# Performance work log

Measured on AMD Instinct MI355X. Metric: run time of the kernel, lower is better.

## Reference

```python
import jax, jax.numpy as jnp
import numpy as np

NUM_PATCHES = 16
FILTER_SIZE = 4
IN_CHANNELS = 64
OUT_CHANNELS = 256
BATCH = 64


def setup_inputs() -> dict:
    key = jax.random.key(0)
    k1, k2 = jax.random.split(key)
    D = NUM_PATCHES * FILTER_SIZE
    x = jax.random.normal(k1, (BATCH, IN_CHANNELS, D, D), dtype=jnp.float32)
    w = jax.random.normal(
        k2,
        (OUT_CHANNELS, IN_CHANNELS, NUM_PATCHES, NUM_PATCHES, FILTER_SIZE ** 2),
        dtype=jnp.float32,
    )
    return {"x": x, "w": w}


def reference(x, w):
    # x: (N, C, D, D) with D = P*f ; w: (O, C, P, P, f^2)
    N, C, D, _ = x.shape
    O, _, P, _, f2 = w.shape
    f = int(round(f2 ** 0.5))
    # non-overlapping unfold: (N,C,P,f,P,f) -> (N,C,P,P,f,f) -> (N,C,P,P,f^2)
    patches = x.reshape(N, C, P, f, P, f).transpose(0, 1, 2, 4, 3, 5).reshape(N, C, P, P, f2)
    # locally-connected contraction over in_channels and filter elements
    y = jnp.einsum('ncpqf,ocpqf->nopq', patches, w)
    scale = 1.0 / jnp.sqrt(jnp.asarray(f2 * C, dtype=x.dtype))
    return jax.nn.relu(y * scale)
```

## Files before the change

### kernel.cpp

```cpp
#include <hip/hip_runtime.h>


typedef short bf16x8 __attribute__((ext_vector_type(8)));
typedef float f32x4  __attribute__((ext_vector_type(4)));

__device__ __forceinline__ short f2bf(float f) {
    union { float f; unsigned u; } v; v.f = f;
    return (short)((v.u + 0x7FFFu + ((v.u >> 16) & 1u)) >> 16);
}

__device__ __forceinline__ bf16x8 pack8(f32x4 a, f32x4 b) {
    bf16x8 r;
    r[0] = f2bf(a[0]); r[1] = f2bf(a[1]); r[2] = f2bf(a[2]); r[3] = f2bf(a[3]);
    r[4] = f2bf(b[0]); r[5] = f2bf(b[1]); r[6] = f2bf(b[2]); r[7] = f2bf(b[3]);
    return r;
}

__device__ __forceinline__ void gload16(const void* g, void* l) {
    __builtin_amdgcn_global_load_lds(
        (const __attribute__((address_space(1))) void*)g,
        (__attribute__((address_space(3))) void*)l, 16, 0, 0);
}

__global__ __launch_bounds__(512)
void locblock_fused(const float* __restrict__ x, const float* __restrict__ w,
                    float* __restrict__ out) {
    __shared__ __align__(16) char smem[3][49152];

    const int hw = blockIdx.x;
    const int lb = (hw & 7) * 32 + (hw >> 3);
    const int p  = lb >> 4;
    const int q2 = (lb >> 1) & 7;
    const int oh = lb & 1;

    const int tid  = (int)threadIdx.x;
    const int lane = tid & 63;
    const int wv   = tid >> 6;
    const int l15  = lane & 15;
    const int kq   = lane >> 4;
    const int qw   = wv & 1;
    const int nc   = wv >> 1;

    const float* xsrc[2];
#pragma unroll
    for (int j = 0; j < 2; ++j) {
        const int id = j * 512 + tid;
        const int n = id >> 4, s = id & 15;
        const int u = s ^ (n & 15);
        xsrc[j] = x + (size_t)n * 262144u + (size_t)(u >> 3) * 4096u
                    + (size_t)(4 * p + ((u >> 1) & 3)) * 64u
                    + (size_t)(q2 * 8 + (u & 1) * 4);
    }
    const float* wsrc[4];
#pragma unroll
    for (int j = 0; j < 4; ++j) {
        const int id = j * 512 + tid;
        const int ol = id >> 4, s = id & 15;
        const int u = s ^ (ol & 15);
        wsrc[j] = w + (size_t)(oh * 128 + ol) * 262144u + (size_t)(u >> 3) * 4096u
                    + (size_t)p * 256u + (size_t)(q2 * 32) + (size_t)((u & 7) * 4);
    }

    int aoff[4][2], boff[2][2];
#pragma unroll
    for (int mf = 0; mf < 4; ++mf) {
        const int n = mf * 16 + l15;
        const int v1 = (kq >> 1) * 8 + (kq & 1) * 4 + qw;
        aoff[mf][0] = n * 256 + ((v1       ^ l15) * 16);
        aoff[mf][1] = n * 256 + (((v1 + 2) ^ l15) * 16);
    }
#pragma unroll
    for (int nf = 0; nf < 2; ++nf) {
        const int ol = nc * 32 + nf * 16 + l15;
        const int u1 = (kq >> 1) * 8 + qw * 4 + (kq & 1) * 2;
        boff[nf][0] = 16384 + ol * 256 + ((u1       ^ l15) * 16);
        boff[nf][1] = 16384 + ol * 256 + (((u1 + 1) ^ l15) * 16);
    }

    f32x4 acc[4][2];
#pragma unroll
    for (int mf = 0; mf < 4; ++mf)
#pragma unroll
        for (int nf = 0; nf < 2; ++nf)
            acc[mf][nf] = (f32x4){0.f, 0.f, 0.f, 0.f};

    auto stage = [&](int t, int buf) {
        char* base = smem[buf];
        const size_t toff = (size_t)t * 8192u;
#pragma unroll
        for (int j = 0; j < 2; ++j)
            gload16(xsrc[j] + toff, base + j * 8192 + wv * 1024);
#pragma unroll
        for (int j = 0; j < 4; ++j)
            gload16(wsrc[j] + toff, base + 16384 + j * 8192 + wv * 1024);
    };

    auto compute = [&](int buf) {
        const char* Lb = smem[buf];
        bf16x8 av[4], bv[2];
#pragma unroll
        for (int mf = 0; mf < 4; ++mf)
            av[mf] = pack8(*(const f32x4*)(Lb + aoff[mf][0]),
                           *(const f32x4*)(Lb + aoff[mf][1]));
#pragma unroll
        for (int nf = 0; nf < 2; ++nf)
            bv[nf] = pack8(*(const f32x4*)(Lb + boff[nf][0]),
                           *(const f32x4*)(Lb + boff[nf][1]));
#pragma unroll
        for (int mf = 0; mf < 4; ++mf)
#pragma unroll
            for (int nf = 0; nf < 2; ++nf)
                acc[mf][nf] = __builtin_amdgcn_mfma_f32_16x16x32_bf16(
                    av[mf], bv[nf], acc[mf][nf], 0, 0, 0);
    };

    stage(0, 0);
    stage(1, 1);
    stage(2, 2);
#pragma unroll 1
    for (int t = 0; t < 29; ++t) {
        const int buf = t % 3;
        asm volatile("s_waitcnt vmcnt(12)" ::: "memory");
        __builtin_amdgcn_s_barrier();
        compute(buf);
        asm volatile("s_waitcnt lgkmcnt(0)" ::: "memory");
        __builtin_amdgcn_s_barrier();
        stage(t + 3, buf);
    }
    asm volatile("s_waitcnt vmcnt(12)" ::: "memory");
    __builtin_amdgcn_s_barrier();
    compute(2);
    asm volatile("s_waitcnt vmcnt(6)" ::: "memory");
    __builtin_amdgcn_s_barrier();
    compute(0);
    asm volatile("s_waitcnt vmcnt(0)" ::: "memory");
    __builtin_amdgcn_s_barrier();
    compute(1);

    const float scale = 0.03125f;
    const int pq = p * 16 + q2 * 2 + qw;
#pragma unroll
    for (int mf = 0; mf < 4; ++mf)
#pragma unroll
        for (int nf = 0; nf < 2; ++nf) {
            const int o = oh * 128 + nc * 32 + nf * 16 + l15;
            float* ob = out + (size_t)(mf * 16 + kq * 4) * 65536u
                            + (size_t)o * 256u + pq;
#pragma unroll
            for (int j = 0; j < 4; ++j)
                ob[(size_t)j * 65536u] = fmaxf(acc[mf][nf][j] * scale, 0.0f);
        }
}

extern "C" void kernel_launch(void* const* d_in, const int* in_sizes, int n_in,
                              void* d_out, int out_size, void* d_ws, size_t ws_size,
                              hipStream_t stream) {
    const float* x = (const float*)d_in[0];
    const float* w = (const float*)d_in[1];
    float* out = (float*)d_out;
    locblock_fused<<<dim3(256), dim3(512), 0, stream>>>(x, w, out);
}
```

Before: 95.54 us.

## Retile locally-connected GEMM per patch row with f16 MFMA and LDS-staged output

Each block now handles one patch row p, 32 batch items and 32 output channels across all 16 q positions, instead of a (p, q-pair, o-half) tile. Inputs are loaded as contiguous 1 KB rows per (n or o, channel) into a double-buffered 64 KB LDS stage, iterating over all 64 channels. Each wave computes two q positions using f16 16x16x16 MFMA with a simple truncating conversion, replacing the bf16 16x16x32 path and its manual rounding. Results go through an LDS transpose so global stores become float4 writes contiguous in q. This trades a shallower pipeline and smaller per-wave tiles for more coalesced loads and stores, and f16 conversion could overflow for large inputs.

New measurement: 94.25 us. About the same (-1.4%).

```diff
diff --git a/kernel.cpp b/kernel.cpp
--- a/kernel.cpp
+++ b/kernel.cpp
@@ -1,20 +1,8 @@
 #include <hip/hip_runtime.h>
 
 
-typedef short bf16x8 __attribute__((ext_vector_type(8)));
-typedef float f32x4  __attribute__((ext_vector_type(4)));
-
-__device__ __forceinline__ short f2bf(float f) {
-    union { float f; unsigned u; } v; v.f = f;
-    return (short)((v.u + 0x7FFFu + ((v.u >> 16) & 1u)) >> 16);
-}
-
-__device__ __forceinline__ bf16x8 pack8(f32x4 a, f32x4 b) {
-    bf16x8 r;
-    r[0] = f2bf(a[0]); r[1] = f2bf(a[1]); r[2] = f2bf(a[2]); r[3] = f2bf(a[3]);
-    r[4] = f2bf(b[0]); r[5] = f2bf(b[1]); r[6] = f2bf(b[2]); r[7] = f2bf(b[3]);
-    return r;
-}
+typedef float    f32x4 __attribute__((ext_vector_type(4)));
+typedef _Float16 f16x4 __attribute__((ext_vector_type(4)));
 
 __device__ __forceinline__ void gload16(const void* g, void* l) {
     __builtin_amdgcn_global_load_lds(
@@ -22,134 +10,149 @@
         (__attribute__((address_space(3))) void*)l, 16, 0, 0);
 }
 
+__device__ __forceinline__ f16x4 cvt4(f32x4 v) {
+    f16x4 r;
+    r[0] = (_Float16)v[0]; r[1] = (_Float16)v[1];
+    r[2] = (_Float16)v[2]; r[3] = (_Float16)v[3];
+    return r;
+}
+
 __global__ __launch_bounds__(512)
 void locblock_fused(const float* __restrict__ x, const float* __restrict__ w,
                     float* __restrict__ out) {
-    __shared__ __align__(16) char smem[3][49152];
+    __shared__ __align__(16) char smem[131072];
 
     const int hw = blockIdx.x;
     const int lb = (hw & 7) * 32 + (hw >> 3);
     const int p  = lb >> 4;
-    const int q2 = (lb >> 1) & 7;
-    const int oh = lb & 1;
+    const int og = (lb >> 1) & 7;
+    const int nh = lb & 1;
 
     const int tid  = (int)threadIdx.x;
     const int lane = tid & 63;
     const int wv   = tid >> 6;
     const int l15  = lane & 15;
     const int kq   = lane >> 4;
-    const int qw   = wv & 1;
-    const int nc   = wv >> 1;
 
-    const float* xsrc[2];
-#pragma unroll
-    for (int j = 0; j < 2; ++j) {
-        const int id = j * 512 + tid;
-        const int n = id >> 4, s = id & 15;
-        const int u = s ^ (n & 15);
-        xsrc[j] = x + (size_t)n * 262144u + (size_t)(u >> 3) * 4096u
-                    + (size_t)(4 * p + ((u >> 1) & 3)) * 64u
-                    + (size_t)(q2 * 8 + (u & 1) * 4);
-    }
+    const int u = lane ^ wv;
+    const float* xsrc[4];
     const float* wsrc[4];
 #pragma unroll
     for (int j = 0; j < 4; ++j) {
-        const int id = j * 512 + tid;
-        const int ol = id >> 4, s = id & 15;
-        const int u = s ^ (ol & 15);
-        wsrc[j] = w + (size_t)(oh * 128 + ol) * 262144u + (size_t)(u >> 3) * 4096u
-                    + (size_t)p * 256u + (size_t)(q2 * 32) + (size_t)((u & 7) * 4);
+        xsrc[j] = x + (size_t)(nh * 32 + j * 8 + wv) * 262144u
+                    + (size_t)p * 256u + (size_t)(u * 4);
+        wsrc[j] = w + (size_t)(og * 32 + j * 8 + wv) * 262144u
+                    + (size_t)p * 256u + (size_t)(u * 4);
     }
 
-    int aoff[4][2], boff[2][2];
+    int aoff[2][2], boff[2][2];
 #pragma unroll
-    for (int mf = 0; mf < 4; ++mf) {
-        const int n = mf * 16 + l15;
-        const int v1 = (kq >> 1) * 8 + (kq & 1) * 4 + qw;
-        aoff[mf][0] = n * 256 + ((v1       ^ l15) * 16);
-        aoff[mf][1] = n * 256 + (((v1 + 2) ^ l15) * 16);
-    }
+    for (int qi = 0; qi < 2; ++qi) {
+        const int q = wv * 2 + qi;
 #pragma unroll
-    for (int nf = 0; nf < 2; ++nf) {
-        const int ol = nc * 32 + nf * 16 + l15;
-        const int u1 = (kq >> 1) * 8 + qw * 4 + (kq & 1) * 2;
-        boff[nf][0] = 16384 + ol * 256 + ((u1       ^ l15) * 16);
-        boff[nf][1] = 16384 + ol * 256 + (((u1 + 1) ^ l15) * 16);
+        for (int mf = 0; mf < 2; ++mf)
+            aoff[qi][mf] = (mf * 16 + l15) * 1024
+                         + (((kq * 16 + q) ^ (l15 & 7)) * 16);
+#pragma unroll
+        for (int nf = 0; nf < 2; ++nf)
+            boff[qi][nf] = 32768 + (nf * 16 + l15) * 1024
+                         + (((q * 4 + kq) ^ (l15 & 7)) * 16);
     }
 
-    f32x4 acc[4][2];
+    f32x4 acc[2][2][2];
 #pragma unroll
-    for (int mf = 0; mf < 4; ++mf)
+    for (int qi = 0; qi < 2; ++qi)
 #pragma unroll
-        for (int nf = 0; nf < 2; ++nf)
-            acc[mf][nf] = (f32x4){0.f, 0.f, 0.f, 0.f};
+        for (int mf = 0; mf < 2; ++mf)
+#pragma unroll
+            for (int nf = 0; nf < 2; ++nf)
+                acc[qi][mf][nf] = (f32x4){0.f, 0.f, 0.f, 0.f};
 
-    auto stage = [&](int t, int buf) {
-        char* base = smem[buf];
-        const size_t toff = (size_t)t * 8192u;
-#pragma unroll
-        for (int j = 0; j < 2; ++j)
-            gload16(xsrc[j] + toff, base + j * 8192 + wv * 1024);
+    auto stage = [&](int c) {
+        char* base = smem + (size_t)(c & 1) * 65536u;
+        const size_t coff = (size_t)c * 4096u;
 #pragma unroll
         for (int j = 0; j < 4; ++j)
-            gload16(wsrc[j] + toff, base + 16384 + j * 8192 + wv * 1024);
+            gload16(xsrc[j] + coff, base + (j * 8 + wv) * 1024);
+#pragma unroll
+        for (int j = 0; j < 4; ++j)
+            gload16(wsrc[j] + coff, base + 32768 + (j * 8 + wv) * 1024);
     };
 
-    auto compute = [&](int buf) {
-        const char* Lb = smem[buf];
-        bf16x8 av[4], bv[2];
+    auto compute = [&](int c) {
+        const char* base = smem + (size_t)(c & 1) * 65536u;
 #pragma unroll
-        for (int mf = 0; mf < 4; ++mf)
-            av[mf] = pack8(*(const f32x4*)(Lb + aoff[mf][0]),
-                           *(const f32x4*)(Lb + aoff[mf][1]));
+        for (int qi = 0; qi < 2; ++qi) {
+            f16x4 av[2], bv[2];
 #pragma unroll
-        for (int nf = 0; nf < 2; ++nf)
-            bv[nf] = pack8(*(const f32x4*)(Lb + boff[nf][0]),
-                           *(const f32x4*)(Lb + boff[nf][1]));
-#pragma unroll
-        for (int mf = 0; mf < 4; ++mf)
+            for (int mf = 0; mf < 2; ++mf)
+                av[mf] = cvt4(*(const f32x4*)(base + aoff[qi][mf]));
 #pragma unroll
             for (int nf = 0; nf < 2; ++nf)
-                acc[mf][nf] = __builtin_amdgcn_mfma_f32_16x16x32_bf16(
-                    av[mf], bv[nf], acc[mf][nf], 0, 0, 0);
+                bv[nf] = cvt4(*(const f32x4*)(base + boff[qi][nf]));
+#pragma unroll
+            for (int mf = 0; mf < 2; ++mf)
+#pragma unroll
+                for (int nf = 0; nf < 2; ++nf)
+                    acc[qi][mf][nf] = __builtin_amdgcn_mfma_f32_16x16x16f16(
+                        av[mf], bv[nf], acc[qi][mf][nf], 0, 0, 0);
+        }
     };
 
-    stage(0, 0);
-    stage(1, 1);
-    stage(2, 2);
+    stage(0);
+    stage(1);
 #pragma unroll 1
-    for (int t = 0; t < 29; ++t) {
-        const int buf = t % 3;
-        asm volatile("s_waitcnt vmcnt(12)" ::: "memory");
+    for (int c = 0; c < 62; ++c) {
+        asm volatile("s_waitcnt vmcnt(8)" ::: "memory");
         __builtin_amdgcn_s_barrier();
-        compute(buf);
+        compute(c);
         asm volatile("s_waitcnt lgkmcnt(0)" ::: "memory");
         __builtin_amdgcn_s_barrier();
-        stage(t + 3, buf);
+        stage(c + 2);
     }
-    asm volatile("s_waitcnt vmcnt(12)" ::: "memory");
+    asm volatile("s_waitcnt vmcnt(8)" ::: "memory");
     __builtin_amdgcn_s_barrier();
-    compute(2);
-    asm volatile("s_waitcnt vmcnt(6)" ::: "memory");
-    __builtin_amdgcn_s_barrier();
-    compute(0);
+    compute(62);
     asm volatile("s_waitcnt vmcnt(0)" ::: "memory");
     __builtin_amdgcn_s_barrier();
-    compute(1);
+    compute(63);
 
+    __syncthreads();
+
+    float* T = (float*)smem;
     const float scale = 0.03125f;
-    const int pq = p * 16 + q2 * 2 + qw;
 #pragma unroll
-    for (int mf = 0; mf < 4; ++mf)
+    for (int qi = 0; qi < 2; ++qi) {
+        const int q = wv * 2 + qi;
 #pragma unroll
-        for (int nf = 0; nf < 2; ++nf) {
-            const int o = oh * 128 + nc * 32 + nf * 16 + l15;
-            float* ob = out + (size_t)(mf * 16 + kq * 4) * 65536u
-                            + (size_t)o * 256u + pq;
+        for (int mf = 0; mf < 2; ++mf)
 #pragma unroll
-            for (int j = 0; j < 4; ++j)
-                ob[(size_t)j * 65536u] = fmaxf(acc[mf][nf][j] * scale, 0.0f);
-        }
+            for (int nf = 0; nf < 2; ++nf) {
+                f32x4 r;
+#pragma unroll
+                for (int j = 0; j < 4; ++j)
+                    r[j] = fmaxf(acc[qi][mf][nf][j] * scale, 0.0f);
+                *(f32x4*)(T + q * 1152 + (nf * 16 + l15) * 36
+                            + mf * 16 + kq * 4) = r;
+            }
+    }
+    __syncthreads();
+
+#pragma unroll
+    for (int i = 0; i < 8; ++i) {
+        const int item = i * 512 + tid;
+        const int o  = item >> 7;
+        const int rm = item & 127;
+        const int n  = rm >> 2;
+        const int qg = rm & 3;
+        f32x4 r;
+#pragma unroll
+        for (int s = 0; s < 4; ++s)
+            r[s] = T[(qg * 4 + s) * 1152 + o * 36 + n];
+        *(f32x4*)(out + (size_t)(nh * 32 + n) * 65536u
+                      + (size_t)(og * 32 + o) * 256u
+                      + (size_t)(p * 16 + qg * 4)) = r;
+    }
 }
 
 extern "C" void kernel_launch(void* const* d_in, const int* in_sizes, int n_in,
```

## Retile blocks to 4 q-positions x 64 outputs, double-buffer, stage epilogue via LDS

Applied to the files above, without the earlier changes.

Each block's tile changes from 2 q-positions x 128 output channels to 4 q-positions x 64 output channels. The x-tile per stage doubles while the w-tile stays the same size. The LDS pipeline drops from three buffers to two larger 64KB buffers, which shortens the prefetch depth. The epilogue now transposes results through LDS so each thread writes contiguous 16-byte float4 stores along q, replacing scattered scalar stores. This trades less pipelining depth and an extra LDS round-trip for coalesced output writes and a different x/w reuse balance.

Result: faster. 86.41 us (-9.6%).

```diff
diff --git a/kernel.cpp b/kernel.cpp
--- a/kernel.cpp
+++ b/kernel.cpp
@@ -25,56 +25,61 @@
 __global__ __launch_bounds__(512)
 void locblock_fused(const float* __restrict__ x, const float* __restrict__ w,
                     float* __restrict__ out) {
-    __shared__ __align__(16) char smem[3][49152];
+    __shared__ __align__(16) char smem[131072];
 
     const int hw = blockIdx.x;
     const int lb = (hw & 7) * 32 + (hw >> 3);
     const int p  = lb >> 4;
-    const int q2 = (lb >> 1) & 7;
-    const int oh = lb & 1;
+    const int q4 = (lb >> 2) & 3;
+    const int oq = lb & 3;
 
     const int tid  = (int)threadIdx.x;
     const int lane = tid & 63;
     const int wv   = tid >> 6;
     const int l15  = lane & 15;
     const int kq   = lane >> 4;
-    const int qw   = wv & 1;
-    const int nc   = wv >> 1;
+    const int qiw  = wv >> 1;
+    const int ow   = wv & 1;
 
-    const float* xsrc[2];
+    const float* xsrc[4];
 #pragma unroll
-    for (int j = 0; j < 2; ++j) {
+    for (int j = 0; j < 4; ++j) {
         const int id = j * 512 + tid;
-        const int n = id >> 4, s = id & 15;
+        const int n = id >> 5, s = id & 31;
         const int u = s ^ (n & 15);
-        xsrc[j] = x + (size_t)n * 262144u + (size_t)(u >> 3) * 4096u
-                    + (size_t)(4 * p + ((u >> 1) & 3)) * 64u
-                    + (size_t)(q2 * 8 + (u & 1) * 4);
+        xsrc[j] = x + (size_t)n * 262144u + (size_t)(u >> 4) * 4096u
+                    + (size_t)(4 * p + ((u >> 2) & 3)) * 64u
+                    + (size_t)(q4 * 16 + (u & 3) * 4);
     }
     const float* wsrc[4];
 #pragma unroll
     for (int j = 0; j < 4; ++j) {
         const int id = j * 512 + tid;
-        const int ol = id >> 4, s = id & 15;
-        const int u = s ^ (ol & 15);
-        wsrc[j] = w + (size_t)(oh * 128 + ol) * 262144u + (size_t)(u >> 3) * 4096u
-                    + (size_t)p * 256u + (size_t)(q2 * 32) + (size_t)((u & 7) * 4);
+        const int o = id >> 5, s = id & 31;
+        const int u = s ^ (o & 15);
+        wsrc[j] = w + (size_t)(oq * 64 + o) * 262144u + (size_t)(u >> 4) * 4096u
+                    + (size_t)p * 256u + (size_t)(q4 * 64) + (size_t)((u & 15) * 4);
     }
 
     int aoff[4][2], boff[2][2];
+    {
+        const int coff = kq >> 1, fr0 = (kq & 1) * 2;
 #pragma unroll
-    for (int mf = 0; mf < 4; ++mf) {
-        const int n = mf * 16 + l15;
-        const int v1 = (kq >> 1) * 8 + (kq & 1) * 4 + qw;
-        aoff[mf][0] = n * 256 + ((v1       ^ l15) * 16);
-        aoff[mf][1] = n * 256 + (((v1 + 2) ^ l15) * 16);
-    }
+        for (int mf = 0; mf < 4; ++mf) {
+            const int n = mf * 16 + l15;
 #pragma unroll
-    for (int nf = 0; nf < 2; ++nf) {
-        const int ol = nc * 32 + nf * 16 + l15;
-        const int u1 = (kq >> 1) * 8 + qw * 4 + (kq & 1) * 2;
-        boff[nf][0] = 16384 + ol * 256 + ((u1       ^ l15) * 16);
-        boff[nf][1] = 16384 + ol * 256 + (((u1 + 1) ^ l15) * 16);
+            for (int d = 0; d < 2; ++d)
+                aoff[mf][d] = n * 512
+                    + (coff * 16 + (((fr0 + d) * 4 + qiw) ^ l15)) * 16;
+        }
+#pragma unroll
+        for (int nf = 0; nf < 2; ++nf) {
+            const int o = ow * 32 + nf * 16 + l15;
+#pragma unroll
+            for (int e = 0; e < 2; ++e)
+                boff[nf][e] = 32768 + o * 512
+                    + (coff * 16 + ((qiw * 4 + (kq & 1) * 2 + e) ^ l15)) * 16;
+        }
     }
 
     f32x4 acc[4][2];
@@ -84,19 +89,19 @@
         for (int nf = 0; nf < 2; ++nf)
             acc[mf][nf] = (f32x4){0.f, 0.f, 0.f, 0.f};
 
-    auto stage = [&](int t, int buf) {
-        char* base = smem[buf];
+    auto stage = [&](int t) {
+        char* base = smem + (size_t)(t & 1) * 65536u;
         const size_t toff = (size_t)t * 8192u;
 #pragma unroll
-        for (int j = 0; j < 2; ++j)
-            gload16(xsrc[j] + toff, base + j * 8192 + wv * 1024);
+        for (int j = 0; j < 4; ++j)
+            gload16(xsrc[j] + toff, base + j * 8192 + tid * 16);
 #pragma unroll
         for (int j = 0; j < 4; ++j)
-            gload16(wsrc[j] + toff, base + 16384 + j * 8192 + wv * 1024);
+            gload16(wsrc[j] + toff, base + 32768 + j * 8192 + tid * 16);
     };
 
-    auto compute = [&](int buf) {
-        const char* Lb = smem[buf];
+    auto compute = [&](int t) {
+        const char* Lb = smem + (size_t)(t & 1) * 65536u;
         bf16x8 av[4], bv[2];
 #pragma unroll
         for (int mf = 0; mf < 4; ++mf)
@@ -114,42 +119,53 @@
                     av[mf], bv[nf], acc[mf][nf], 0, 0, 0);
     };
 
-    stage(0, 0);
-    stage(1, 1);
-    stage(2, 2);
+    stage(0);
+    stage(1);
 #pragma unroll 1
-    for (int t = 0; t < 29; ++t) {
-        const int buf = t % 3;
-        asm volatile("s_waitcnt vmcnt(12)" ::: "memory");
+    for (int t = 0; t < 30; ++t) {
+        asm volatile("s_waitcnt vmcnt(8)" ::: "memory");
         __builtin_amdgcn_s_barrier();
-        compute(buf);
+        compute(t);
         asm volatile("s_waitcnt lgkmcnt(0)" ::: "memory");
         __builtin_amdgcn_s_barrier();
-        stage(t + 3, buf);
+        stage(t + 2);
     }
-    asm volatile("s_waitcnt vmcnt(12)" ::: "memory");
+    asm volatile("s_waitcnt vmcnt(8)" ::: "memory");
     __builtin_amdgcn_s_barrier();
-    compute(2);
-    asm volatile("s_waitcnt vmcnt(6)" ::: "memory");
-    __builtin_amdgcn_s_barrier();
-    compute(0);
+    compute(30);
     asm volatile("s_waitcnt vmcnt(0)" ::: "memory");
     __builtin_amdgcn_s_barrier();
-    compute(1);
+    compute(31);
 
+    __syncthreads();
+
+    float* T = (float*)smem;
     const float scale = 0.03125f;
-    const int pq = p * 16 + q2 * 2 + qw;
 #pragma unroll
     for (int mf = 0; mf < 4; ++mf)
 #pragma unroll
         for (int nf = 0; nf < 2; ++nf) {
-            const int o = oh * 128 + nc * 32 + nf * 16 + l15;
-            float* ob = out + (size_t)(mf * 16 + kq * 4) * 65536u
-                            + (size_t)o * 256u + pq;
+            const int o  = ow * 32 + nf * 16 + l15;
+            const int n0 = mf * 16 + kq * 4;
+            f32x4 r;
 #pragma unroll
             for (int j = 0; j < 4; ++j)
-                ob[(size_t)j * 65536u] = fmaxf(acc[mf][nf][j] * scale, 0.0f);
+                r[j] = fmaxf(acc[mf][nf][j] * scale, 0.0f);
+            *(f32x4*)(T + (size_t)(qiw * 64 + o) * 72u + n0) = r;
         }
+    __syncthreads();
+
+#pragma unroll
+    for (int i = 0; i < 8; ++i) {
+        const int item = i * 512 + tid;
+        const int n = item >> 6, o = item & 63;
+        f32x4 r;
+#pragma unroll
+        for (int s = 0; s < 4; ++s)
+            r[s] = T[(size_t)(s * 64 + o) * 72u + n];
+        *(f32x4*)(out + (size_t)n * 65536u + (size_t)(oq * 64 + o) * 256u
+                      + (size_t)(p * 16 + q4 * 4)) = r;
+    }
 }
 
 extern "C" void kernel_launch(void* const* d_in, const int* in_sizes, int n_in,
```
